# Performance work log

Measured on AMD Instinct MI355X. Metric: run time of the kernel, lower is better.

Reference implementation:

```python
import jax, jax.numpy as jnp
import numpy as np

N_NODES = 100000
N_EDGES = 1250000
IN_CH, HID_CH, OUT_CH = 128, 64, 40


def setup_inputs() -> dict:
    key = jax.random.key(0)
    ks = jax.random.split(key, 8)
    x = jax.random.normal(ks[0], (N_NODES, IN_CH), dtype=jnp.float32)
    edge_index = jax.random.randint(ks[1], (2, N_EDGES), 0, N_NODES, dtype=jnp.int64)
    # Glorot-ish scaled weights
    W1 = jax.random.normal(ks[2], (IN_CH, HID_CH), dtype=jnp.float32) * (1.0 / np.sqrt(IN_CH))
    b1 = jnp.zeros((HID_CH,), dtype=jnp.float32)
    W2 = jax.random.normal(ks[3], (HID_CH, HID_CH), dtype=jnp.float32) * (1.0 / np.sqrt(HID_CH))
    b2 = jnp.zeros((HID_CH,), dtype=jnp.float32)
    W3 = jax.random.normal(ks[4], (HID_CH, OUT_CH), dtype=jnp.float32) * (1.0 / np.sqrt(HID_CH))
    b3 = jnp.zeros((OUT_CH,), dtype=jnp.float32)
    return {"x": x, "edge_index": edge_index, "W1": W1, "b1": b1,
            "W2": W2, "b2": b2, "W3": W3, "b3": b3}


def reference(x, edge_index, W1, b1, W2, b2, W3, b3):
    n = x.shape[0]
    # PyG GCNConv: add self-loops, symmetric deg^-1/2 normalization
    loop = jnp.arange(n, dtype=edge_index.dtype)
    src = jnp.concatenate([edge_index[0], loop])  # [E+N]
    dst = jnp.concatenate([edge_index[1], loop])
    deg = jax.ops.segment_sum(jnp.ones_like(dst, dtype=x.dtype), dst, num_segments=n)
    dinv = jnp.where(deg > 0, jax.lax.rsqrt(deg), 0.0)
    coef = (dinv[src] * dinv[dst])[:, None]  # [E+N, 1]

    def conv(h, W, b):
        h = h @ W                                  # [N, F_out]
        msg = h[src] * coef                        # gather + scale: [E+N, F_out]
        return jax.ops.segment_sum(msg, dst, num_segments=n) + b

    h = jax.nn.relu(conv(x, W1, b1))   # dropout is identity in eval mode
    h = jax.nn.relu(conv(h, W2, b2))
    h = conv(h, W3, b3)
    return jax.nn.log_softmax(h, axis=1)
```

## Files before the change

kernel.cpp:

```cpp
#include <hip/hip_runtime.h>
#include <hip/hip_fp16.h>

#define NN 100000
#define NE 1250000
#define NBIN 512
#define RBIN 196
#define PAD 16
#define CAP 4096
#define EPB 4096
#define EPT 16
#define BCAP 3072

__device__ __forceinline__ int eidx(const int* __restrict__ e32, int f, int i){
    return f ? e32[2*(size_t)i] : e32[i];
}

__device__ __forceinline__ void scan_bins(const int* __restrict__ cnts, int* __restrict__ boff){
    if(threadIdx.x < 64){
        int b0 = threadIdx.x*8;
        int pre[8]; int run = 0;
        #pragma unroll
        for(int i = 0; i < 8; ++i){ pre[i] = run; run += cnts[(b0+i)*PAD]; }
        int inc = run;
        for(int o = 1; o < 64; o <<= 1){
            int u = __shfl_up(inc, o, 64);
            if(threadIdx.x >= (unsigned)o) inc += u;
        }
        int excl = inc - run;
        #pragma unroll
        for(int i = 0; i < 8; ++i) boff[b0+i] = excl + pre[i];
    }
    __syncthreads();
}

__global__ __launch_bounds__(256) void binC_k(const int* __restrict__ e32,
                                              int* __restrict__ binCur, int2* __restrict__ bins){
    __shared__ int2 ST[EPB];
    __shared__ int hist[NBIN];
    __shared__ int lstart[NBIN];
    __shared__ int gbase[NBIN];
    __shared__ int cur[NBIN];
    __shared__ int flg;
    const int t = threadIdx.x;
    const int e0 = blockIdx.x * EPB;
    const int n = min(EPB, NE - e0);

    for(int b = t; b < NBIN; b += 256){ hist[b] = 0; cur[b] = 0; }
    if(t < 64){
        int v = e32[2*t + 1];
        unsigned long long b = __ballot(v != 0);
        if(t == 0) flg = (b == 0ULL) ? 1 : 0;
    }
    __syncthreads();
    const int f = flg;

    int2 ed[EPT];
    #pragma unroll
    for(int k = 0; k < EPT; ++k){
        int i = k*256 + t;
        if(i < n){
            ed[k].x = eidx(e32, f, e0 + i);
            ed[k].y = eidx(e32, f, NE + e0 + i);
            atomicAdd(&hist[ed[k].y / RBIN], 1);
        }
    }
    __syncthreads();

    if(t < 64){
        int b0 = t*8;
        int pre[8]; int run = 0;
        #pragma unroll
        for(int i = 0; i < 8; ++i){ pre[i] = run; run += hist[b0 + i]; }
        int inc = run;
        for(int o = 1; o < 64; o <<= 1){
            int u = __shfl_up(inc, o, 64);
            if(t >= o) inc += u;
        }
        int excl = inc - run;
        #pragma unroll
        for(int i = 0; i < 8; ++i) lstart[b0 + i] = excl + pre[i];
    }
    for(int b = t; b < NBIN; b += 256) gbase[b] = b*BCAP + atomicAdd(&binCur[b*PAD], hist[b]);
    __syncthreads();

    #pragma unroll
    for(int k = 0; k < EPT; ++k){
        int i = k*256 + t;
        if(i < n){
            int b = ed[k].y / RBIN;
            int lo = atomicAdd(&cur[b], 1);
            ST[lstart[b] + lo] = ed[k];
        }
    }
    __syncthreads();

    for(int i = t; i < n; i += 256){
        int2 e = ST[i];
        int b = e.y / RBIN;
        bins[gbase[b] + (i - lstart[b])] = e;
    }
}

__global__ __launch_bounds__(256) void binD_k(const int2* __restrict__ bins, const int* __restrict__ binCur,
                                              int* __restrict__ rp, float* __restrict__ dinv,
                                              int* __restrict__ csr_src){
    __shared__ int2 ES[CAP];
    __shared__ int hist[256];
    __shared__ int sc[256];
    __shared__ int cur[256];
    __shared__ int boff[NBIN];
    const int b = blockIdx.x;
    const int t = threadIdx.x;
    if(b == NBIN-1 && t == 0) rp[NN] = NE;
    const int nbase = b * RBIN;
    if(nbase >= NN) return;
    const int nend = min(nbase + RBIN, NN);
    const int nr = nend - nbase;
    hist[t] = 0; cur[t] = 0;
    __syncthreads();
    scan_bins(binCur, boff);
    const int off0 = boff[b];
    const int rb   = b * BCAP;
    const int cnt  = binCur[b*PAD];

    const bool single = (cnt <= CAP);
    for(int c0 = 0; c0 < cnt; c0 += CAP){
        int n = min(CAP, cnt - c0);
        for(int i = t; i < n; i += 256) ES[i] = bins[rb + c0 + i];
        __syncthreads();
        for(int i = t; i < n; i += 256) atomicAdd(&hist[ES[i].y - nbase], 1);
        __syncthreads();
    }
    int v = hist[t];
    sc[t] = v; __syncthreads();
    for(int off = 1; off < 256; off <<= 1){
        int u = (t >= off) ? sc[t - off] : 0;
        __syncthreads();
        sc[t] += u;
        __syncthreads();
    }
    int excl = sc[t] - v;
    sc[t] = excl;
    if(t < nr){
        rp[nbase + t]   = off0 + excl;
        dinv[nbase + t] = rsqrtf((float)(v + 1));
    }
    __syncthreads();
    for(int c0 = 0; c0 < cnt; c0 += CAP){
        int n = min(CAP, cnt - c0);
        if(!single){
            for(int i = t; i < n; i += 256) ES[i] = bins[rb + c0 + i];
            __syncthreads();
        }
        for(int i = t; i < n; i += 256){
            int dl = ES[i].y - nbase;
            int p = atomicAdd(&cur[dl], 1);
            csr_src[off0 + sc[dl] + p] = ES[i].x;
        }
        if(!single) __syncthreads();
    }
}

template<bool AHALF, int K, int NC, int KT, int OSTR, bool RELU>
__global__ __launch_bounds__(256) void gemm_k(const void* __restrict__ Araw, const float* __restrict__ W,
                                              const float* __restrict__ dinv,
                                              __half* __restrict__ out, int M){
    constexpr int CHT = KT/4;
    constexpr int CMASK = CHT - 1;
    __shared__ float Xs[64*KT];
    __shared__ float Ws[KT*NC];
    const int tid  = threadIdx.x;
    const int base = blockIdx.x * 64;
    const int tx = tid & 15, ty = tid >> 4;
    const int c0 = tx * 4;
    float acc[4][4] = {};

    for(int k0 = 0; k0 < K; k0 += KT){
        {
            const float4* Wv = (const float4*)(W + k0*NC);
            float4* Wsv = (float4*)Ws;
            for(int i = tid; i < KT*NC/4; i += 256) Wsv[i] = Wv[i];
        }
        {
            const int ch = tid & (CHT - 1);
            const int r0 = tid / CHT;
            constexpr int RSTEP = 256 / CHT;
            #pragma unroll
            for(int r = r0; r < 64; r += RSTEP){
                int row = base + r; if(row >= M) row = M - 1;
                float4 v;
                if(AHALF){
                    const __half2* ap = (const __half2*)((const __half*)Araw + (size_t)row*K + k0 + ch*4);
                    float2 fa = __half22float2(ap[0]), fb = __half22float2(ap[1]);
                    v = make_float4(fa.x, fa.y, fb.x, fb.y);
                } else {
                    v = *(const float4*)((const float*)Araw + (size_t)row*K + k0 + ch*4);
                }
                if(RELU){ v.x=fmaxf(v.x,0.f); v.y=fmaxf(v.y,0.f); v.z=fmaxf(v.z,0.f); v.w=fmaxf(v.w,0.f); }
                int sw = (ch + r) & CMASK;
                *(float4*)&Xs[r*KT + sw*4] = v;
            }
        }
        __syncthreads();

        if(c0 < NC){
            for(int k4 = 0; k4 < CHT; ++k4){
                float4 xs[4];
                #pragma unroll
                for(int i = 0; i < 4; ++i){
                    int r = ty*4 + i;
                    int sw = (k4 + r) & CMASK;
                    xs[i] = *(const float4*)&Xs[r*KT + (sw << 2)];
                }
                float4 wsv[4];
                #pragma unroll
                for(int kk = 0; kk < 4; ++kk) wsv[kk] = *(const float4*)&Ws[(k4*4 + kk)*NC + c0];
                #pragma unroll
                for(int kk = 0; kk < 4; ++kk){
                    const float* wp = (const float*)&wsv[kk];
                    #pragma unroll
                    for(int i = 0; i < 4; ++i){
                        float xv = ((const float*)&xs[i])[kk];
                        #pragma unroll
                        for(int j = 0; j < 4; ++j) acc[i][j] += xv * wp[j];
                    }
                }
            }
        }
        __syncthreads();
    }
    #pragma unroll
    for(int i = 0; i < 4; ++i){
        int row = base + ty*4 + i;
        if(row < M && c0 < NC){
            float dv = dinv[row];
            __half2 h01 = __floats2half2_rn(acc[i][0]*dv, acc[i][1]*dv);
            __half2 h23 = __floats2half2_rn(acc[i][2]*dv, acc[i][3]*dv);
            __half2* dst = (__half2*)&out[(size_t)row*OSTR + c0];
            dst[0] = h01;
            dst[1] = h23;
        }
    }
}

__global__ __launch_bounds__(256) void agg64_k(const __half* __restrict__ P, const int* __restrict__ rp,
                                               const int* __restrict__ csr_src,
                                               const float* __restrict__ dinv, const float* __restrict__ bias,
                                               __half* __restrict__ G){
    constexpr unsigned F2 = 32;
    const int lane = threadIdx.x & 63;
    const int v = (blockIdx.x*256 + threadIdx.x) >> 6;
    if(v >= NN) return;
    const int g = lane >> 4;
    const int q = lane & 15;
    const unsigned qo = (unsigned)q*2;
    const __half2* __restrict__ P2 = (const __half2*)P;

    const int beg = rp[v], end = rp[v + 1];
    float4 acc = make_float4(0.f, 0.f, 0.f, 0.f);
    if(g == 0){
        __half2 a = P2[(unsigned)v*F2 + qo], b = P2[(unsigned)v*F2 + qo + 1];
        float2 fa = __half22float2(a), fb = __half22float2(b);
        acc = make_float4(fa.x, fa.y, fb.x, fb.y);
    }

    int j = beg;
    #pragma unroll 1
    for(; j + 16 <= end; j += 16){
        unsigned i0 = (unsigned)csr_src[j + g]     *F2 + qo;
        unsigned i1 = (unsigned)csr_src[j + 4 + g] *F2 + qo;
        unsigned i2 = (unsigned)csr_src[j + 8 + g] *F2 + qo;
        unsigned i3 = (unsigned)csr_src[j + 12 + g]*F2 + qo;
        __half2 a0 = P2[i0], b0 = P2[i0+1];
        __half2 a1 = P2[i1], b1 = P2[i1+1];
        __half2 a2 = P2[i2], b2 = P2[i2+1];
        __half2 a3 = P2[i3], b3 = P2[i3+1];
        __half2 sa = __hadd2(a0, a1), sb = __hadd2(b0, b1);
        __half2 ta = __hadd2(a2, a3), tb = __hadd2(b2, b3);
        float2 f0 = __half22float2(sa), f1 = __half22float2(sb);
        float2 f2 = __half22float2(ta), f3 = __half22float2(tb);
        acc.x += f0.x + f2.x; acc.y += f0.y + f2.y;
        acc.z += f1.x + f3.x; acc.w += f1.y + f3.y;
    }
    if(j + 8 <= end){
        unsigned i0 = (unsigned)csr_src[j + g]    *F2 + qo;
        unsigned i1 = (unsigned)csr_src[j + 4 + g]*F2 + qo;
        __half2 a0 = P2[i0], b0 = P2[i0+1];
        __half2 a1 = P2[i1], b1 = P2[i1+1];
        __half2 sa = __hadd2(a0, a1), sb = __hadd2(b0, b1);
        float2 f0 = __half22float2(sa), f1 = __half22float2(sb);
        acc.x += f0.x; acc.y += f0.y; acc.z += f1.x; acc.w += f1.y;
        j += 8;
    }
    if(j + 4 <= end){
        unsigned i0 = (unsigned)csr_src[j + g]*F2 + qo;
        __half2 a = P2[i0], b = P2[i0+1];
        float2 fa = __half22float2(a), fb = __half22float2(b);
        acc.x += fa.x; acc.y += fa.y; acc.z += fb.x; acc.w += fb.y;
        j += 4;
    }
    const int rem = end - j;
    if(g < rem){
        unsigned i0 = (unsigned)csr_src[j + g]*F2 + qo;
        __half2 a = P2[i0], b = P2[i0+1];
        float2 fa = __half22float2(a), fb = __half22float2(b);
        acc.x += fa.x; acc.y += fa.y; acc.z += fb.x; acc.w += fb.y;
    }

    #pragma unroll
    for(int m = 16; m <= 32; m <<= 1){
        acc.x += __shfl_xor(acc.x, m, 64);
        acc.y += __shfl_xor(acc.y, m, 64);
        acc.z += __shfl_xor(acc.z, m, 64);
        acc.w += __shfl_xor(acc.w, m, 64);
    }

    if(g == 0){
        const float d = dinv[v];
        float4 bb = *(const float4*)&bias[q*4];
        __half2 h01 = __floats2half2_rn(fmaf(acc.x, d, bb.x), fmaf(acc.y, d, bb.y));
        __half2 h23 = __floats2half2_rn(fmaf(acc.z, d, bb.z), fmaf(acc.w, d, bb.w));
        __half2* dst = (__half2*)&G[(size_t)v*64 + q*4];
        dst[0] = h01;
        dst[1] = h23;
    }
}

__global__ __launch_bounds__(256) void agg40_k(const __half* __restrict__ P, const int* __restrict__ rp,
                                               const int* __restrict__ csr_src,
                                               const float* __restrict__ dinv, const float* __restrict__ bias,
                                               float* __restrict__ G){
    constexpr int NQ = 10;
    constexpr unsigned F2 = 32;
    const int lane = threadIdx.x & 63;
    const int v = (blockIdx.x*256 + threadIdx.x) >> 6;
    if(v >= NN) return;
    const int g = lane >> 4;
    const int q = lane & 15;
    const bool qa = (q < NQ);
    const unsigned qo = (unsigned)q*2;
    const __half2* __restrict__ P2 = (const __half2*)P;

    const int beg = rp[v], end = rp[v + 1];
    float4 acc = make_float4(0.f, 0.f, 0.f, 0.f);
    if(g == 0 && qa){
        __half2 a = P2[(unsigned)v*F2 + qo], b = P2[(unsigned)v*F2 + qo + 1];
        float2 fa = __half22float2(a), fb = __half22float2(b);
        acc = make_float4(fa.x, fa.y, fb.x, fb.y);
    }

    int j = beg;
    #pragma unroll 1
    for(; j + 8 <= end; j += 8){
        unsigned i0 = (unsigned)csr_src[j + g]    *F2 + qo;
        unsigned i1 = (unsigned)csr_src[j + 4 + g]*F2 + qo;
        __half2 a0 = P2[i0], b0 = P2[i0+1];
        __half2 a1 = P2[i1], b1 = P2[i1+1];
        __half2 sa = __hadd2(a0, a1), sb = __hadd2(b0, b1);
        float2 f0 = __half22float2(sa), f1 = __half22float2(sb);
        acc.x += f0.x; acc.y += f0.y; acc.z += f1.x; acc.w += f1.y;
    }
    if(j + 4 <= end){
        unsigned i0 = (unsigned)csr_src[j + g]*F2 + qo;
        __half2 a = P2[i0], b = P2[i0+1];
        float2 fa = __half22float2(a), fb = __half22float2(b);
        acc.x += fa.x; acc.y += fa.y; acc.z += fb.x; acc.w += fb.y;
        j += 4;
    }
    const int rem = end - j;
    if(g < rem){
        unsigned i0 = (unsigned)csr_src[j + g]*F2 + qo;
        __half2 a = P2[i0], b = P2[i0+1];
        float2 fa = __half22float2(a), fb = __half22float2(b);
        acc.x += fa.x; acc.y += fa.y; acc.z += fb.x; acc.w += fb.y;
    }

    #pragma unroll
    for(int m = 16; m <= 32; m <<= 1){
        acc.x += __shfl_xor(acc.x, m, 64);
        acc.y += __shfl_xor(acc.y, m, 64);
        acc.z += __shfl_xor(acc.z, m, 64);
        acc.w += __shfl_xor(acc.w, m, 64);
    }

    float4 r;
    const float d = dinv[v];
    if(g == 0 && qa){
        float4 bb = *(const float4*)&bias[q*4];
        r.x = fmaf(acc.x, d, bb.x);
        r.y = fmaf(acc.y, d, bb.y);
        r.z = fmaf(acc.z, d, bb.z);
        r.w = fmaf(acc.w, d, bb.w);
    }
    float lm = (g == 0 && qa) ? fmaxf(fmaxf(r.x, r.y), fmaxf(r.z, r.w)) : -3.402823466e38f;
    #pragma unroll
    for(int m = 1; m <= 8; m <<= 1) lm = fmaxf(lm, __shfl_xor(lm, m, 64));
    float ls = (g == 0 && qa)
             ? (__expf(r.x - lm) + __expf(r.y - lm) + __expf(r.z - lm) + __expf(r.w - lm)) : 0.0f;
    #pragma unroll
    for(int m = 1; m <= 8; m <<= 1) ls += __shfl_xor(ls, m, 64);
    if(g == 0 && qa){
        float lz = lm + __logf(ls);
        r.x -= lz; r.y -= lz; r.z -= lz; r.w -= lz;
        *(float4*)&G[(size_t)v*40 + q*4] = r;
    }
}

extern "C" void kernel_launch(void* const* d_in, const int* in_sizes, int n_in,
                              void* d_out, int out_size, void* d_ws, size_t ws_size,
                              hipStream_t stream){
    const float* x   = (const float*)d_in[0];
    const int*   e32 = (const int*)  d_in[1];
    const float* W1  = (const float*)d_in[2];
    const float* b1  = (const float*)d_in[3];
    const float* W2  = (const float*)d_in[4];
    const float* b2  = (const float*)d_in[5];
    const float* W3  = (const float*)d_in[6];
    const float* b3  = (const float*)d_in[7];
    float* out = (float*)d_out;

    char* ws = (char*)d_ws;
    size_t off = 0;
    auto alloc = [&](size_t bytes) -> void* {
        void* p = ws + off;
        off = (off + bytes + 255) & ~(size_t)255;
        return p;
    };
    int*    binCur = (int*)   alloc((size_t)NBIN*PAD*4);
    int*    rp     = (int*)   alloc((size_t)(NN+1)*4);
    float*  dinv   = (float*) alloc((size_t)NN*4);
    int*    csr_s  = (int*)   alloc((size_t)NE*4);
    __half* ph     = (__half*)alloc((size_t)NN*64*2);
    __half* gA     = (__half*)alloc((size_t)NN*64*2);
    __half* gB     = (__half*)alloc((size_t)NN*64*2);
    int2*   bins   = (int2*)  alloc((size_t)NBIN*BCAP*8);

    hipMemsetAsync(binCur, 0, (size_t)NBIN*PAD*4, stream);
    binC_k<<<(NE + EPB - 1)/EPB, 256, 0, stream>>>(e32, binCur, bins);
    binD_k<<<NBIN, 256, 0, stream>>>(bins, binCur, rp, dinv, csr_s);

    const int GEMM_GRID = (NN + 63)/64;
    const int AGG_GRID  = (NN*64 + 255)/256;

    gemm_k<false,128,64,64,64,false><<<GEMM_GRID, 256, 0, stream>>>(x,  W1, dinv, ph, NN);
    agg64_k<<<AGG_GRID, 256, 0, stream>>>(ph, rp, csr_s, dinv, b1, gA);
    gemm_k<true, 64,64,64,64,true ><<<GEMM_GRID, 256, 0, stream>>>(gA, W2, dinv, ph, NN);
    agg64_k<<<AGG_GRID, 256, 0, stream>>>(ph, rp, csr_s, dinv, b2, gB);
    gemm_k<true, 64,40,64,64,true ><<<GEMM_GRID, 256, 0, stream>>>(gB, W3, dinv, ph, NN);
    agg40_k<<<AGG_GRID, 256, 0, stream>>>(ph, rp, csr_s, dinv, b3, out);
}
```

Measured before the change: 244.7 us.

## Split first-layer aggregation into four source-range passes for cache locality

Within each destination row, the CSR build now sorts edges into four buckets keyed by source node range (src>>15) and records per-bucket offsets in a new rp4 array. The first aggregation runs as four kernels, each gathering only from one quarter of the source feature table so the working set fits in cache better. Partial sums go through a half-precision scratch buffer. This adds three extra launches and extra read/write traffic for the partials, plus rounding of intermediate sums to half precision.

```diff
diff --git a/kernel.cpp b/kernel.cpp
--- a/kernel.cpp
+++ b/kernel.cpp
@@ -102,12 +102,13 @@
 }
 
 __global__ __launch_bounds__(256) void binD_k(const int2* __restrict__ bins, const int* __restrict__ binCur,
-                                              int* __restrict__ rp, float* __restrict__ dinv,
-                                              int* __restrict__ csr_src){
+                                              int* __restrict__ rp, int* __restrict__ rp4,
+                                              float* __restrict__ dinv, int* __restrict__ csr_src){
     __shared__ int2 ES[CAP];
-    __shared__ int hist[256];
-    __shared__ int sc[256];
-    __shared__ int cur[256];
+    __shared__ int hist[1024];
+    __shared__ int scx[1024];
+    __shared__ int cur[1024];
+    __shared__ int red[256];
     __shared__ int boff[NBIN];
     const int b = blockIdx.x;
     const int t = threadIdx.x;
@@ -116,7 +117,7 @@
     if(nbase >= NN) return;
     const int nend = min(nbase + RBIN, NN);
     const int nr = nend - nbase;
-    hist[t] = 0; cur[t] = 0;
+    for(int i = t; i < 1024; i += 256){ hist[i] = 0; cur[i] = 0; }
     __syncthreads();
     scan_bins(binCur, boff);
     const int off0 = boff[b];
@@ -128,22 +129,30 @@
         int n = min(CAP, cnt - c0);
         for(int i = t; i < n; i += 256) ES[i] = bins[rb + c0 + i];
         __syncthreads();
-        for(int i = t; i < n; i += 256) atomicAdd(&hist[ES[i].y - nbase], 1);
+        for(int i = t; i < n; i += 256)
+            atomicAdd(&hist[(ES[i].y - nbase)*4 + (ES[i].x >> 15)], 1);
         __syncthreads();
     }
-    int v = hist[t];
-    sc[t] = v; __syncthreads();
+    int h0 = hist[t*4], h1 = hist[t*4+1], h2 = hist[t*4+2], h3 = hist[t*4+3];
+    int run = h0 + h1 + h2 + h3;
+    red[t] = run; __syncthreads();
     for(int off = 1; off < 256; off <<= 1){
-        int u = (t >= off) ? sc[t - off] : 0;
+        int u = (t >= off) ? red[t - off] : 0;
         __syncthreads();
-        sc[t] += u;
+        red[t] += u;
         __syncthreads();
     }
-    int excl = sc[t] - v;
-    sc[t] = excl;
+    int ebase = red[t] - run;
+    scx[t*4]   = ebase;
+    scx[t*4+1] = ebase + h0;
+    scx[t*4+2] = ebase + h0 + h1;
+    scx[t*4+3] = ebase + h0 + h1 + h2;
     if(t < nr){
-        rp[nbase + t]   = off0 + excl;
-        dinv[nbase + t] = rsqrtf((float)(v + 1));
+        rp[nbase + t] = off0 + ebase;
+        int4 w = make_int4(off0 + ebase, off0 + ebase + h0,
+                           off0 + ebase + h0 + h1, off0 + ebase + h0 + h1 + h2);
+        *(int4*)&rp4[(size_t)(nbase + t)*4] = w;
+        dinv[nbase + t] = rsqrtf((float)(run + 1));
     }
     __syncthreads();
     for(int c0 = 0; c0 < cnt; c0 += CAP){
@@ -153,9 +162,9 @@
             __syncthreads();
         }
         for(int i = t; i < n; i += 256){
-            int dl = ES[i].y - nbase;
-            int p = atomicAdd(&cur[dl], 1);
-            csr_src[off0 + sc[dl] + p] = ES[i].x;
+            int k = (ES[i].y - nbase)*4 + (ES[i].x >> 15);
+            int p = atomicAdd(&cur[k], 1);
+            csr_src[off0 + scx[k] + p] = ES[i].x;
         }
         if(!single) __syncthreads();
     }
@@ -243,28 +252,9 @@
     }
 }
 
-__global__ __launch_bounds__(256) void agg64_k(const __half* __restrict__ P, const int* __restrict__ rp,
-                                               const int* __restrict__ csr_src,
-                                               const float* __restrict__ dinv, const float* __restrict__ bias,
-                                               __half* __restrict__ G){
+__device__ __forceinline__ void gather64(const __half2* __restrict__ P2, const int* __restrict__ csr_src,
+                                         int j, int end, int g, unsigned qo, float4& acc){
     constexpr unsigned F2 = 32;
-    const int lane = threadIdx.x & 63;
-    const int v = (blockIdx.x*256 + threadIdx.x) >> 6;
-    if(v >= NN) return;
-    const int g = lane >> 4;
-    const int q = lane & 15;
-    const unsigned qo = (unsigned)q*2;
-    const __half2* __restrict__ P2 = (const __half2*)P;
-
-    const int beg = rp[v], end = rp[v + 1];
-    float4 acc = make_float4(0.f, 0.f, 0.f, 0.f);
-    if(g == 0){
-        __half2 a = P2[(unsigned)v*F2 + qo], b = P2[(unsigned)v*F2 + qo + 1];
-        float2 fa = __half22float2(a), fb = __half22float2(b);
-        acc = make_float4(fa.x, fa.y, fb.x, fb.y);
-    }
-
-    int j = beg;
     #pragma unroll 1
     for(; j + 16 <= end; j += 16){
         unsigned i0 = (unsigned)csr_src[j + g]     *F2 + qo;
@@ -306,6 +296,29 @@
         float2 fa = __half22float2(a), fb = __half22float2(b);
         acc.x += fa.x; acc.y += fa.y; acc.z += fb.x; acc.w += fb.y;
     }
+}
+
+__global__ __launch_bounds__(256) void agg64_k(const __half* __restrict__ P, const int* __restrict__ rp,
+                                               const int* __restrict__ csr_src,
+                                               const float* __restrict__ dinv, const float* __restrict__ bias,
+                                               __half* __restrict__ G){
+    constexpr unsigned F2 = 32;
+    const int lane = threadIdx.x & 63;
+    const int v = (blockIdx.x*256 + threadIdx.x) >> 6;
+    if(v >= NN) return;
+    const int g = lane >> 4;
+    const int q = lane & 15;
+    const unsigned qo = (unsigned)q*2;
+    const __half2* __restrict__ P2 = (const __half2*)P;
+
+    const int beg = rp[v], end = rp[v + 1];
+    float4 acc = make_float4(0.f, 0.f, 0.f, 0.f);
+    if(g == 0){
+        __half2 a = P2[(unsigned)v*F2 + qo], b = P2[(unsigned)v*F2 + qo + 1];
+        float2 fa = __half22float2(a), fb = __half22float2(b);
+        acc = make_float4(fa.x, fa.y, fb.x, fb.y);
+    }
+    gather64(P2, csr_src, beg, end, g, qo, acc);
 
     #pragma unroll
     for(int m = 16; m <= 32; m <<= 1){
@@ -323,6 +336,64 @@
         __half2* dst = (__half2*)&G[(size_t)v*64 + q*4];
         dst[0] = h01;
         dst[1] = h23;
+    }
+}
+
+template<int C>
+__global__ __launch_bounds__(256) void agg64c_k(const __half* __restrict__ P, const int* __restrict__ rp,
+                                                const int* __restrict__ rp4, const int* __restrict__ csr_src,
+                                                const float* __restrict__ dinv, const float* __restrict__ bias,
+                                                __half* __restrict__ Gpart, __half* __restrict__ G){
+    constexpr bool FIRST = (C == 0), LAST = (C == 3);
+    constexpr unsigned F2 = 32;
+    const int lane = threadIdx.x & 63;
+    const int v = (blockIdx.x*256 + threadIdx.x) >> 6;
+    if(v >= NN) return;
+    const int g = lane >> 4;
+    const int q = lane & 15;
+    const unsigned qo = (unsigned)q*2;
+    const __half2* __restrict__ P2 = (const __half2*)P;
+
+    int4 s4 = *(const int4*)&rp4[(size_t)v*4];
+    int beg = (C == 0) ? s4.x : (C == 1) ? s4.y : (C == 2) ? s4.z : s4.w;
+    int end;
+    if(LAST) end = rp[v + 1];
+    else     end = (C == 0) ? s4.y : (C == 1) ? s4.z : s4.w;
+
+    float4 acc = make_float4(0.f, 0.f, 0.f, 0.f);
+    if(LAST && g == 0){
+        __half2 a = P2[(unsigned)v*F2 + qo], b = P2[(unsigned)v*F2 + qo + 1];
+        float2 fa = __half22float2(a), fb = __half22float2(b);
+        acc = make_float4(fa.x, fa.y, fb.x, fb.y);
+    }
+    gather64(P2, csr_src, beg, end, g, qo, acc);
+
+    #pragma unroll
+    for(int m = 16; m <= 32; m <<= 1){
+        acc.x += __shfl_xor(acc.x, m, 64);
+        acc.y += __shfl_xor(acc.y, m, 64);
+        acc.z += __shfl_xor(acc.z, m, 64);
+        acc.w += __shfl_xor(acc.w, m, 64);
+    }
+
+    if(g == 0){
+        __half2* gp = (__half2*)&Gpart[(size_t)v*64 + q*4];
+        if(!FIRST){
+            float2 p0 = __half22float2(gp[0]), p1 = __half22float2(gp[1]);
+            acc.x += p0.x; acc.y += p0.y; acc.z += p1.x; acc.w += p1.y;
+        }
+        if(!LAST){
+            gp[0] = __floats2half2_rn(acc.x, acc.y);
+            gp[1] = __floats2half2_rn(acc.z, acc.w);
+        } else {
+            const float d = dinv[v];
+            float4 bb = *(const float4*)&bias[q*4];
+            __half2 h01 = __floats2half2_rn(fmaf(acc.x, d, bb.x), fmaf(acc.y, d, bb.y));
+            __half2 h23 = __floats2half2_rn(fmaf(acc.z, d, bb.z), fmaf(acc.w, d, bb.w));
+            __half2* dst = (__half2*)&G[(size_t)v*64 + q*4];
+            dst[0] = h01;
+            dst[1] = h23;
+        }
     }
 }
 
@@ -428,6 +499,7 @@
     };
     int*    binCur = (int*)   alloc((size_t)NBIN*PAD*4);
     int*    rp     = (int*)   alloc((size_t)(NN+1)*4);
+    int*    rp4    = (int*)   alloc((size_t)NN*4*4);
     float*  dinv   = (float*) alloc((size_t)NN*4);
     int*    csr_s  = (int*)   alloc((size_t)NE*4);
     __half* ph     = (__half*)alloc((size_t)NN*64*2);
@@ -437,13 +509,16 @@
 
     hipMemsetAsync(binCur, 0, (size_t)NBIN*PAD*4, stream);
     binC_k<<<(NE + EPB - 1)/EPB, 256, 0, stream>>>(e32, binCur, bins);
-    binD_k<<<NBIN, 256, 0, stream>>>(bins, binCur, rp, dinv, csr_s);
+    binD_k<<<NBIN, 256, 0, stream>>>(bins, binCur, rp, rp4, dinv, csr_s);
 
     const int GEMM_GRID = (NN + 63)/64;
     const int AGG_GRID  = (NN*64 + 255)/256;
 
     gemm_k<false,128,64,64,64,false><<<GEMM_GRID, 256, 0, stream>>>(x,  W1, dinv, ph, NN);
-    agg64_k<<<AGG_GRID, 256, 0, stream>>>(ph, rp, csr_s, dinv, b1, gA);
+    agg64c_k<0><<<AGG_GRID, 256, 0, stream>>>(ph, rp, rp4, csr_s, dinv, b1, gB, gA);
+    agg64c_k<1><<<AGG_GRID, 256, 0, stream>>>(ph, rp, rp4, csr_s, dinv, b1, gB, gA);
+    agg64c_k<2><<<AGG_GRID, 256, 0, stream>>>(ph, rp, rp4, csr_s, dinv, b1, gB, gA);
+    agg64c_k<3><<<AGG_GRID, 256, 0, stream>>>(ph, rp, rp4, csr_s, dinv, b1, gB, gA);
     gemm_k<true, 64,64,64,64,true ><<<GEMM_GRID, 256, 0, stream>>>(gA, W2, dinv, ph, NN);
     agg64_k<<<AGG_GRID, 256, 0, stream>>>(ph, rp, csr_s, dinv, b2, gB);
     gemm_k<true, 64,40,64,64,true ><<<GEMM_GRID, 256, 0, stream>>>(gB, W3, dinv, ph, NN);
```

Result: slower. 307.8 us (+25.8%).
